# Kernel tuning notes

Hardware: AMD Instinct MI355X
Metric: run time of the kernel (lower is better)

## Reference

```python
import jax, jax.numpy as jnp
import numpy as np

N, D, K = 500000, 64, 256
INIT_COUNT = 100  # torch module initializes counts to 100 per cluster


def setup_inputs() -> dict:
    key = jax.random.key(0)
    k1, k2 = jax.random.split(key)
    embedded = jax.random.normal(k1, (N, D), dtype=jnp.float32)
    centers = jax.random.normal(k2, (K, D), dtype=jnp.float32)
    counts = jnp.ones((K,), dtype=jnp.int32) * INIT_COUNT
    return {"embedded": embedded, "centers": centers, "counts": counts}


def reference(embedded, centers, counts):
    # predict_hard: squared euclidean cdist + argmin over clusters
    x2 = jnp.sum(embedded * embedded, axis=1, keepdims=True)          # [N,1]
    c2 = jnp.sum(centers * centers, axis=1)                           # [K]
    dist = x2 - 2.0 * jnp.einsum('nd,kd->nk', embedded, centers) + c2  # [N,K]
    labels = jnp.argmin(dist, axis=1).astype(jnp.int32)               # [N]

    # dcn_loss: gather assigned center, squared diff, sum / N
    diff = embedded - centers[labels]                                 # [N,D]
    loss = jnp.sum(diff * diff) / embedded.shape[0]

    # update_centroids: the sequential running-mean update
    #   center = (1 - 1/count) * center + (1/count) * x  (count incremented per sample)
    # telescopes exactly to a segment-sum form:
    #   new_center_c = (counts_old[c]*center_c + sum_{i: label_i=c} x_i) / (counts_old[c] + n_c)
    n_clusters = centers.shape[0]
    seg_sum = jax.ops.segment_sum(embedded, labels, num_segments=n_clusters)  # [K,D]
    seg_cnt = jax.ops.segment_sum(jnp.ones_like(labels), labels, num_segments=n_clusters)  # [K] int32
    new_counts = counts + seg_cnt
    old_w = counts.astype(embedded.dtype)[:, None]
    new_w = new_counts.astype(embedded.dtype)[:, None]
    new_centers = (old_w * centers + seg_sum) / new_w
    return labels, loss, new_centers, new_counts
```

## Files before the change

kernel.cpp:

```cpp
#include <hip/hip_runtime.h>


typedef __attribute__((ext_vector_type(8))) short bf16x8;
typedef __attribute__((ext_vector_type(4))) float f32x4;

constexpr int K = 256;
constexpr int D = 64;
constexpr int BLK = 768;
constexpr int GRID = 256;
constexpr int WPB = BLK / 64;

struct alignas(16) PackW { unsigned int w[4]; };

__device__ __forceinline__ unsigned int pack_hi(unsigned int a, unsigned int b) {
  return (a >> 16) | (b & 0xffff0000u);
}

__device__ __forceinline__ void split8(const float4 a, const float4 b,
                                       bf16x8& s0, bf16x8& s1) {
  PackW p0, p1;
  const float fa[8] = {a.x, a.y, a.z, a.w, b.x, b.y, b.z, b.w};
#pragma unroll
  for (int i = 0; i < 4; ++i) {
    float f0 = fa[2 * i], f1 = fa[2 * i + 1];
    unsigned u0 = __float_as_uint(f0), u1 = __float_as_uint(f1);
    p0.w[i] = pack_hi(u0, u1);
    float r0 = f0 - __uint_as_float(u0 & 0xffff0000u);
    float r1 = f1 - __uint_as_float(u1 & 0xffff0000u);
    p1.w[i] = pack_hi(__float_as_uint(r0), __float_as_uint(r1));
  }
  s0 = __builtin_bit_cast(bf16x8, p0);
  s1 = __builtin_bit_cast(bf16x8, p1);
}

__global__ __launch_bounds__(BLK, 3) void assign_kernel(
    const float* __restrict__ emb,
    const float* __restrict__ centers,
    float* __restrict__ out_labels,
    float* __restrict__ ws_seg,
    int*   __restrict__ ws_cnt,
    float* __restrict__ ws_loss,
    int N)
{
  __shared__ __align__(16) unsigned short Bls[2 * K * D];
  __shared__ float seg_lds[K * D];
  __shared__ float hneg_lds[K];
  __shared__ int   cnt_lds[K];
  __shared__ float red[WPB];

  const int tid = threadIdx.x;

  for (int e = tid; e < K * D; e += BLK) {
    int j = e >> 6, d = e & 63;
    float cv = centers[e];
    unsigned u = __float_as_uint(cv);
    unsigned short h0 = (unsigned short)(u >> 16);
    float r = cv - __uint_as_float(u & 0xffff0000u);
    unsigned short h1 = (unsigned short)(__float_as_uint(r) >> 16);
    int nt = j >> 4, c = j & 15;
    int si = nt * 1024 + c * 64 + (d ^ ((c & 7) << 3));
    Bls[si] = h0;
    Bls[16384 + si] = h1;
  }
  if (tid < K) {
    const float4* cp = (const float4*)(centers + tid * D);
    float s = 0.f;
#pragma unroll
    for (int q = 0; q < 16; ++q) {
      float4 v = cp[q];
      s = fmaf(v.x, v.x, s); s = fmaf(v.y, v.y, s);
      s = fmaf(v.z, v.z, s); s = fmaf(v.w, v.w, s);
    }
    hneg_lds[tid] = -0.5f * s;
  }
  for (int e = tid; e < K * D; e += BLK) seg_lds[e] = 0.f;
  if (tid < K) cnt_lds[tid] = 0;
  __syncthreads();

  const int lane = tid & 63;
  const int wid  = tid >> 6;
  const int g    = lane >> 4;
  const int cc   = lane & 15;
  const int swzm = (cc & 7) << 3;
  const int bRow = cc * 64;
  const int bk0 = (8 * g) ^ swzm;
  const int bk1 = (32 + 8 * g) ^ swzm;

  float lossAcc = 0.f;
  const int TILES = N >> 5;
  const int waveGid = blockIdx.x * WPB + wid;

  for (int tile = waveGid; tile < TILES; tile += GRID * WPB) {
    const int base = tile << 5;

    float4 xa[2][2][2];
    bf16x8 fx[2][2][2];
    float  x2m[2];
#pragma unroll
    for (int Mt = 0; Mt < 2; ++Mt) {
#pragma unroll
      for (int ks = 0; ks < 2; ++ks) {
        const float4* rp = (const float4*)(emb + (size_t)(base + Mt * 16 + cc) * D + ks * 32 + g * 8);
        xa[Mt][ks][0] = rp[0];
        xa[Mt][ks][1] = rp[1];
      }
#pragma unroll
      for (int ks = 0; ks < 2; ++ks)
        split8(xa[Mt][ks][0], xa[Mt][ks][1], fx[Mt][ks][0], fx[Mt][ks][1]);
      float p = 0.f;
#pragma unroll
      for (int ks = 0; ks < 2; ++ks)
#pragma unroll
        for (int h = 0; h < 2; ++h) {
          float4 v = xa[Mt][ks][h];
          p = fmaf(v.x, v.x, p); p = fmaf(v.y, v.y, p);
          p = fmaf(v.z, v.z, p); p = fmaf(v.w, v.w, p);
        }
      p += __shfl_xor(p, 16);
      p += __shfl_xor(p, 32);
      x2m[Mt] = p;
    }

    float bV[2][4];
    int   bI[2][4];
#pragma unroll
    for (int Mt = 0; Mt < 2; ++Mt)
#pragma unroll
      for (int r = 0; r < 4; ++r) { bV[Mt][r] = -3.0e38f; bI[Mt][r] = 0; }

    f32x4 accP[2];
#pragma unroll
    for (int nt = 0; nt < 16; ++nt) {
      float h = hneg_lds[nt * 16 + cc];
      f32x4 ci = {h, h, h, h};
      f32x4 a0, a1;
      {
        bf16x8 b0 = *(const bf16x8*)&Bls[nt * 1024 + bRow + bk0];
        bf16x8 b1 = *(const bf16x8*)&Bls[16384 + nt * 1024 + bRow + bk0];
        a0 = __builtin_amdgcn_mfma_f32_16x16x32_bf16(fx[0][0][0], b0, ci, 0, 0, 0);
        a0 = __builtin_amdgcn_mfma_f32_16x16x32_bf16(fx[0][0][1], b0, a0, 0, 0, 0);
        a0 = __builtin_amdgcn_mfma_f32_16x16x32_bf16(fx[0][0][0], b1, a0, 0, 0, 0);
        a1 = __builtin_amdgcn_mfma_f32_16x16x32_bf16(fx[1][0][0], b0, ci, 0, 0, 0);
        a1 = __builtin_amdgcn_mfma_f32_16x16x32_bf16(fx[1][0][1], b0, a1, 0, 0, 0);
        a1 = __builtin_amdgcn_mfma_f32_16x16x32_bf16(fx[1][0][0], b1, a1, 0, 0, 0);
      }
      {
        bf16x8 b0 = *(const bf16x8*)&Bls[nt * 1024 + bRow + bk1];
        bf16x8 b1 = *(const bf16x8*)&Bls[16384 + nt * 1024 + bRow + bk1];
        a0 = __builtin_amdgcn_mfma_f32_16x16x32_bf16(fx[0][1][0], b0, a0, 0, 0, 0);
        a0 = __builtin_amdgcn_mfma_f32_16x16x32_bf16(fx[0][1][1], b0, a0, 0, 0, 0);
        a0 = __builtin_amdgcn_mfma_f32_16x16x32_bf16(fx[0][1][0], b1, a0, 0, 0, 0);
        a1 = __builtin_amdgcn_mfma_f32_16x16x32_bf16(fx[1][1][0], b0, a1, 0, 0, 0);
        a1 = __builtin_amdgcn_mfma_f32_16x16x32_bf16(fx[1][1][1], b0, a1, 0, 0, 0);
        a1 = __builtin_amdgcn_mfma_f32_16x16x32_bf16(fx[1][1][0], b1, a1, 0, 0, 0);
      }
      if (nt > 0) {
        int idx0 = (nt - 1) * 16 + cc;
#pragma unroll
        for (int Mt = 0; Mt < 2; ++Mt)
#pragma unroll
          for (int r = 0; r < 4; ++r) {
            float v = accP[Mt][r];
            if (v > bV[Mt][r]) { bV[Mt][r] = v; bI[Mt][r] = idx0; }
          }
      }
      accP[0] = a0; accP[1] = a1;
    }
    {
      int idx0 = 15 * 16 + cc;
#pragma unroll
      for (int Mt = 0; Mt < 2; ++Mt)
#pragma unroll
        for (int r = 0; r < 4; ++r) {
          float v = accP[Mt][r];
          if (v > bV[Mt][r]) { bV[Mt][r] = v; bI[Mt][r] = idx0; }
        }
    }

#pragma unroll
    for (int Mt = 0; Mt < 2; ++Mt)
#pragma unroll
      for (int r = 0; r < 4; ++r)
#pragma unroll
        for (int m = 1; m <= 8; m <<= 1) {
          float ov = __shfl_xor(bV[Mt][r], m);
          int   oi = __shfl_xor(bI[Mt][r], m);
          if (ov > bV[Mt][r]) { bV[Mt][r] = ov; bI[Mt][r] = oi; }
        }

#pragma unroll
    for (int Mt = 0; Mt < 2; ++Mt) {
      int i01 = (cc & 1) ? bI[Mt][1] : bI[Mt][0];
      int i23 = (cc & 1) ? bI[Mt][3] : bI[Mt][2];
      int vi  = (cc & 2) ? i23 : i01;
      float v01 = (cc & 1) ? bV[Mt][1] : bV[Mt][0];
      float v23 = (cc & 1) ? bV[Mt][3] : bV[Mt][2];
      float vv  = (cc & 2) ? v23 : v01;
      float x2s = __shfl(x2m[Mt], g * 4 + (cc & 3));
      if (cc < 4) {
        out_labels[base + Mt * 16 + g * 4 + cc] = (float)vi;
        lossAcc += x2s - 2.0f * vv;
        atomicAdd(&cnt_lds[vi], 1);
      }
      int srcl = (cc >> 2) << 4;
      int l0 = __shfl(bI[Mt][0], srcl);
      int l1 = __shfl(bI[Mt][1], srcl);
      int l2 = __shfl(bI[Mt][2], srcl);
      int l3 = __shfl(bI[Mt][3], srcl);
      int t01 = (cc & 1) ? l1 : l0;
      int t23 = (cc & 1) ? l3 : l2;
      int lbl = (cc & 2) ? t23 : t01;
      int sb = lbl << 6;
      int sw = lbl & 31;
#pragma unroll
      for (int ks = 0; ks < 2; ++ks)
#pragma unroll
        for (int hf = 0; hf < 2; ++hf) {
          float4 v = xa[Mt][ks][hf];
          int d0 = ks * 32 + 8 * g + hf * 4;
          atomicAdd(&seg_lds[sb + ((d0 + 0) ^ sw)], v.x);
          atomicAdd(&seg_lds[sb + ((d0 + 1) ^ sw)], v.y);
          atomicAdd(&seg_lds[sb + ((d0 + 2) ^ sw)], v.z);
          atomicAdd(&seg_lds[sb + ((d0 + 3) ^ sw)], v.w);
        }
    }
  }

#pragma unroll
  for (int off = 32; off > 0; off >>= 1) lossAcc += __shfl_down(lossAcc, off);
  if (lane == 0) red[wid] = lossAcc;
  __syncthreads();
  if (tid == 0) {
    float t = 0.f;
#pragma unroll
    for (int w = 0; w < WPB; ++w) t += red[w];
    unsafeAtomicAdd(ws_loss, t);
  }
  for (int e = tid; e < K * D; e += BLK) {
    int k = e >> 6, d = e & 63;
    unsafeAtomicAdd(&ws_seg[e], seg_lds[(k << 6) + (d ^ (k & 31))]);
  }
  if (tid < K) atomicAdd(&ws_cnt[tid], cnt_lds[tid]);
}

__global__ void finalize_kernel(
    const float* __restrict__ centers,
    const int* __restrict__ counts,
    const float* __restrict__ ws_seg,
    const int* __restrict__ ws_cnt,
    const float* __restrict__ ws_loss,
    float* __restrict__ out_loss,
    float* __restrict__ out_centers,
    float* __restrict__ out_counts,
    int N)
{
  int idx = blockIdx.x * blockDim.x + threadIdx.x;
  if (idx < K * D) {
    int k = idx >> 6;
    float oldw = (float)counts[k];
    float neww = (float)(counts[k] + ws_cnt[k]);
    out_centers[idx] = fmaf(oldw, centers[idx], ws_seg[idx]) / neww;
  }
  if (idx < K) out_counts[idx] = (float)(counts[idx] + ws_cnt[idx]);
  if (idx == 0) out_loss[0] = ws_loss[0] / (float)N;
}

extern "C" void kernel_launch(void* const* d_in, const int* in_sizes, int n_in,
                              void* d_out, int out_size, void* d_ws, size_t ws_size,
                              hipStream_t stream) {
  const float* emb     = (const float*)d_in[0];
  const float* centers = (const float*)d_in[1];
  const int*   counts  = (const int*)d_in[2];

  const int Kn = in_sizes[2];
  const int Dn = in_sizes[1] / Kn;
  const int N  = in_sizes[0] / Dn;

  float* out         = (float*)d_out;
  float* out_labels  = out;
  float* out_loss    = out + N;
  float* out_centers = out + N + 1;
  float* out_counts  = out + N + 1 + (size_t)Kn * Dn;

  float* ws_seg  = (float*)d_ws;
  int*   ws_cnt  = (int*)(ws_seg + (size_t)Kn * Dn);
  float* ws_loss = (float*)(ws_cnt + Kn);

  hipMemsetAsync(d_ws, 0, (size_t)(Kn * Dn + Kn + 1) * sizeof(float), stream);

  hipLaunchKernelGGL(assign_kernel, dim3(GRID), dim3(BLK), 0, stream,
                     emb, centers, out_labels, ws_seg, ws_cnt, ws_loss, N);

  hipLaunchKernelGGL(finalize_kernel, dim3((Kn * Dn + 255) / 256), dim3(256), 0, stream,
                     centers, counts, ws_seg, ws_cnt, ws_loss,
                     out_loss, out_centers, out_counts, N);
}
```

Baseline: 442.6 us.

## Pack argmax index into float low bits and use raw ds_add_f32 atomics

Encodes the cluster index in the low 8 mantissa bits of each score so the running argmax and cross-lane reduction become single fmaxf ops instead of compare/select pairs on value and index. It also accumulates per-lane x² into one loss sum instead of reducing it per row with shuffles, caches the center norms in registers, and issues the LDS float atomics as inline ds_add_f32 with explicit addresses. The index packing truncates score precision and can change tie-breaking or near-tie labels relative to exact argmin. The volatile asm also needs an explicit waitcnt before the barrier.

```diff
diff --git a/kernel.cpp b/kernel.cpp
--- a/kernel.cpp
+++ b/kernel.cpp
@@ -11,6 +11,9 @@
 constexpr int WPB = BLK / 64;
 
 struct alignas(16) PackW { unsigned int w[4]; };
+
+#define DS_ADD_F32(addr32, val) \
+  asm volatile("ds_add_f32 %0, %1" :: "v"(addr32), "v"(val))
 
 __device__ __forceinline__ unsigned int pack_hi(unsigned int a, unsigned int b) {
   return (a >> 16) | (b & 0xffff0000u);
@@ -86,7 +89,14 @@
   const int bk0 = (8 * g) ^ swzm;
   const int bk1 = (32 + 8 * g) ^ swzm;
 
-  float lossAcc = 0.f;
+  float hreg[16];
+#pragma unroll
+  for (int nt = 0; nt < 16; ++nt) hreg[nt] = hneg_lds[nt * 16 + cc];
+
+  const unsigned segbase = (unsigned)(size_t)seg_lds;
+
+  float lossS = 0.f;
+  float lossX = 0.f;
   const int TILES = N >> 5;
   const int waveGid = blockIdx.x * WPB + wid;
 
@@ -95,7 +105,6 @@
 
     float4 xa[2][2][2];
     bf16x8 fx[2][2][2];
-    float  x2m[2];
 #pragma unroll
     for (int Mt = 0; Mt < 2; ++Mt) {
 #pragma unroll
@@ -107,31 +116,26 @@
 #pragma unroll
       for (int ks = 0; ks < 2; ++ks)
         split8(xa[Mt][ks][0], xa[Mt][ks][1], fx[Mt][ks][0], fx[Mt][ks][1]);
-      float p = 0.f;
 #pragma unroll
       for (int ks = 0; ks < 2; ++ks)
 #pragma unroll
         for (int h = 0; h < 2; ++h) {
           float4 v = xa[Mt][ks][h];
-          p = fmaf(v.x, v.x, p); p = fmaf(v.y, v.y, p);
-          p = fmaf(v.z, v.z, p); p = fmaf(v.w, v.w, p);
+          lossX = fmaf(v.x, v.x, lossX); lossX = fmaf(v.y, v.y, lossX);
+          lossX = fmaf(v.z, v.z, lossX); lossX = fmaf(v.w, v.w, lossX);
         }
-      p += __shfl_xor(p, 16);
-      p += __shfl_xor(p, 32);
-      x2m[Mt] = p;
-    }
-
-    float bV[2][4];
-    int   bI[2][4];
+    }
+
+    float bE[2][4];
 #pragma unroll
     for (int Mt = 0; Mt < 2; ++Mt)
 #pragma unroll
-      for (int r = 0; r < 4; ++r) { bV[Mt][r] = -3.0e38f; bI[Mt][r] = 0; }
+      for (int r = 0; r < 4; ++r) bE[Mt][r] = -3.0e38f;
 
     f32x4 accP[2];
 #pragma unroll
     for (int nt = 0; nt < 16; ++nt) {
-      float h = hneg_lds[nt * 16 + cc];
+      float h = hreg[nt];
       f32x4 ci = {h, h, h, h};
       f32x4 a0, a1;
       {
@@ -155,25 +159,25 @@
         a1 = __builtin_amdgcn_mfma_f32_16x16x32_bf16(fx[1][1][0], b1, a1, 0, 0, 0);
       }
       if (nt > 0) {
-        int idx0 = (nt - 1) * 16 + cc;
+        unsigned ib = (unsigned)cc | (unsigned)((nt - 1) << 4);
 #pragma unroll
         for (int Mt = 0; Mt < 2; ++Mt)
 #pragma unroll
           for (int r = 0; r < 4; ++r) {
-            float v = accP[Mt][r];
-            if (v > bV[Mt][r]) { bV[Mt][r] = v; bI[Mt][r] = idx0; }
+            unsigned u = (__float_as_uint(accP[Mt][r]) & 0xFFFFFF00u) | ib;
+            bE[Mt][r] = fmaxf(bE[Mt][r], __uint_as_float(u));
           }
       }
       accP[0] = a0; accP[1] = a1;
     }
     {
-      int idx0 = 15 * 16 + cc;
+      unsigned ib = (unsigned)cc | (15u << 4);
 #pragma unroll
       for (int Mt = 0; Mt < 2; ++Mt)
 #pragma unroll
         for (int r = 0; r < 4; ++r) {
-          float v = accP[Mt][r];
-          if (v > bV[Mt][r]) { bV[Mt][r] = v; bI[Mt][r] = idx0; }
+          unsigned u = (__float_as_uint(accP[Mt][r]) & 0xFFFFFF00u) | ib;
+          bE[Mt][r] = fmaxf(bE[Mt][r], __uint_as_float(u));
         }
     }
 
@@ -182,35 +186,30 @@
 #pragma unroll
       for (int r = 0; r < 4; ++r)
 #pragma unroll
-        for (int m = 1; m <= 8; m <<= 1) {
-          float ov = __shfl_xor(bV[Mt][r], m);
-          int   oi = __shfl_xor(bI[Mt][r], m);
-          if (ov > bV[Mt][r]) { bV[Mt][r] = ov; bI[Mt][r] = oi; }
-        }
+        for (int m = 1; m <= 8; m <<= 1)
+          bE[Mt][r] = fmaxf(bE[Mt][r], __shfl_xor(bE[Mt][r], m));
 
 #pragma unroll
     for (int Mt = 0; Mt < 2; ++Mt) {
-      int i01 = (cc & 1) ? bI[Mt][1] : bI[Mt][0];
-      int i23 = (cc & 1) ? bI[Mt][3] : bI[Mt][2];
-      int vi  = (cc & 2) ? i23 : i01;
-      float v01 = (cc & 1) ? bV[Mt][1] : bV[Mt][0];
-      float v23 = (cc & 1) ? bV[Mt][3] : bV[Mt][2];
+      float v01 = (cc & 1) ? bE[Mt][1] : bE[Mt][0];
+      float v23 = (cc & 1) ? bE[Mt][3] : bE[Mt][2];
       float vv  = (cc & 2) ? v23 : v01;
-      float x2s = __shfl(x2m[Mt], g * 4 + (cc & 3));
       if (cc < 4) {
+        int vi = (int)(__float_as_uint(vv) & 255u);
         out_labels[base + Mt * 16 + g * 4 + cc] = (float)vi;
-        lossAcc += x2s - 2.0f * vv;
+        lossS += vv;
         atomicAdd(&cnt_lds[vi], 1);
       }
       int srcl = (cc >> 2) << 4;
-      int l0 = __shfl(bI[Mt][0], srcl);
-      int l1 = __shfl(bI[Mt][1], srcl);
-      int l2 = __shfl(bI[Mt][2], srcl);
-      int l3 = __shfl(bI[Mt][3], srcl);
-      int t01 = (cc & 1) ? l1 : l0;
-      int t23 = (cc & 1) ? l3 : l2;
-      int lbl = (cc & 2) ? t23 : t01;
-      int sb = lbl << 6;
+      float e0 = __shfl(bE[Mt][0], srcl);
+      float e1 = __shfl(bE[Mt][1], srcl);
+      float e2 = __shfl(bE[Mt][2], srcl);
+      float e3 = __shfl(bE[Mt][3], srcl);
+      float t01 = (cc & 1) ? e1 : e0;
+      float t23 = (cc & 1) ? e3 : e2;
+      float er  = (cc & 2) ? t23 : t01;
+      int lbl = (int)(__float_as_uint(er) & 255u);
+      unsigned sb = segbase + ((unsigned)lbl << 8);
       int sw = lbl & 31;
 #pragma unroll
       for (int ks = 0; ks < 2; ++ks)
@@ -218,17 +217,20 @@
         for (int hf = 0; hf < 2; ++hf) {
           float4 v = xa[Mt][ks][hf];
           int d0 = ks * 32 + 8 * g + hf * 4;
-          atomicAdd(&seg_lds[sb + ((d0 + 0) ^ sw)], v.x);
-          atomicAdd(&seg_lds[sb + ((d0 + 1) ^ sw)], v.y);
-          atomicAdd(&seg_lds[sb + ((d0 + 2) ^ sw)], v.z);
-          atomicAdd(&seg_lds[sb + ((d0 + 3) ^ sw)], v.w);
+          DS_ADD_F32(sb + (unsigned)(((d0 + 0) ^ sw) << 2), v.x);
+          DS_ADD_F32(sb + (unsigned)(((d0 + 1) ^ sw) << 2), v.y);
+          DS_ADD_F32(sb + (unsigned)(((d0 + 2) ^ sw) << 2), v.z);
+          DS_ADD_F32(sb + (unsigned)(((d0 + 3) ^ sw) << 2), v.w);
         }
     }
   }
 
-#pragma unroll
-  for (int off = 32; off > 0; off >>= 1) lossAcc += __shfl_down(lossAcc, off);
-  if (lane == 0) red[wid] = lossAcc;
+  asm volatile("s_waitcnt lgkmcnt(0)" ::: "memory");
+
+  float acc = fmaf(-2.f, lossS, lossX);
+#pragma unroll
+  for (int off = 32; off > 0; off >>= 1) acc += __shfl_down(acc, off);
+  if (lane == 0) red[wid] = acc;
   __syncthreads();
   if (tid == 0) {
     float t = 0.f;
```

After: 394.5 us. -10.9%, faster.
